# Kernel tuning notes

Hardware: AMD Instinct MI355X
Metric: run time of the kernel (lower is better)

The kernel has to match this reference:

```python
import jax, jax.numpy as jnp
import numpy as np

D = 1024   # n_embd
H = 16     # n_head
NL = 6     # n_layer
B = 16
L = 64
T = 3 * L  # interleaved (rtg, state, action) tokens
NB = 100   # rtg bucket number
DF = 4 * D


def _ln(x, g, b, eps=1e-5):
    mu = jnp.mean(x, -1, keepdims=True)
    var = jnp.mean((x - mu) ** 2, -1, keepdims=True)
    return (x - mu) * jax.lax.rsqrt(var + eps) * g + b


def _gelu(x):
    return jax.nn.gelu(x, approximate=False)  # matches torch F.gelu (erf)


def setup_inputs() -> dict:
    key = jax.random.key(0)
    ks = iter(jax.random.split(key, 64))
    def rn(shape, s=0.02):
        return jax.random.normal(next(ks), shape, jnp.float32) * s
    inp = dict(
        states=jax.random.normal(next(ks), (B, L, 91), jnp.float32),
        actions=jax.random.normal(next(ks), (B, L, 1, 27), jnp.float32),
        rtgs=jax.random.uniform(next(ks), (B, L), jnp.float32) * 100.0,
        attention_mask=jnp.ones((B, L), bool),
        y_len=L,
        # state encoder: Linear(91,D) GELU Linear(D,D) GELU
        se_w1=rn((91, D)), se_b1=jnp.zeros(D), se_w2=rn((D, D)), se_b2=jnp.zeros(D),
        # action encoder: Linear(27,D) GELU Linear(D,D)
        ae_w1=rn((27, D)), ae_b1=jnp.zeros(D), ae_w2=rn((D, D)), ae_b2=jnp.zeros(D),
        # Autodis
        ad_bucket_w=rn((1, D)), ad_bucket_b=jnp.zeros(D), ad_ret_w=rn((1, NB)), ad_res_w=rn((NB, NB)),
        pos_emb=rn((1, T, D)),
        # transformer blocks (stacked over layers)
        ln1_g=jnp.ones((NL, D)), ln1_b=jnp.zeros((NL, D)),
        Wq=rn((NL, D, D)), bq=jnp.zeros((NL, D)),
        Wk=rn((NL, D, D)), bk=jnp.zeros((NL, D)),
        Wv=rn((NL, D, D)), bv=jnp.zeros((NL, D)),
        Wp=rn((NL, D, D)), bp=jnp.zeros((NL, D)),
        ln2_g=jnp.ones((NL, D)), ln2_b=jnp.zeros((NL, D)),
        Wm1=rn((NL, D, DF)), bm1=jnp.zeros((NL, DF)),
        Wm2=rn((NL, DF, D)), bm2=jnp.zeros((NL, D)),
        lin_w=rn((D, 27)), lin_b=jnp.zeros(27),
    )
    return inp


def _forward(attention_mask, states, actions, rtgs, se_w1, se_b1, se_w2, se_b2,
             ae_w1, ae_b1, ae_w2, ae_b2, ad_bucket_w, ad_bucket_b, ad_ret_w, ad_res_w,
             pos_emb, ln1_g, ln1_b, Wq, bq, Wk, bk, Wv, bv, Wp, bp,
             ln2_g, ln2_b, Wm1, bm1, Wm2, bm2, lin_w, lin_b):
    Bsz, Ls = states.shape[0], states.shape[1]
    Ts = 3 * Ls
    hd = D // H
    # encoders
    state_emb = _gelu(_gelu(states @ se_w1 + se_b1) @ se_w2 + se_b2)          # [B,L,D]
    act = actions[:, :, 0, :]                                                  # squeeze(2) -> [B,L,27]
    action_emb = _gelu(act @ ae_w1 + ae_b1) @ ae_w2 + ae_b2                    # [B,L,D]
    # Autodis rtg embedding
    bucket_value = jnp.linspace(0.0, 100.0, NB).reshape(NB, 1)
    meta = bucket_value @ ad_bucket_w + ad_bucket_b                            # [NB,D]
    s = jax.nn.leaky_relu(rtgs[..., None] @ ad_ret_w)                          # [B,L,NB]
    s = s + s @ ad_res_w
    e = jnp.exp(s - jnp.max(s, -1, keepdims=True))
    p = e / (1e-8 + jnp.sum(e, -1, keepdims=True))
    rtg_emb = p @ meta                                                         # [B,L,D]
    # interleave rtg/state/action tokens -> [B,3L,D]
    tok = jnp.stack([rtg_emb, state_emb, action_emb], axis=2).reshape(Bsz, Ts, D)
    x = tok + pos_emb[:, :Ts]
    # combined padding + causal mask
    m = jnp.repeat(attention_mask, 3, axis=1)                                  # [B,3L]
    causal = jnp.tril(jnp.ones((Ts, Ts), bool))
    fmask = m[:, None, :, None] & m[:, None, None, :] & causal[None, None]     # [B,1,T,T]
    scale = 1.0 / np.sqrt(hd)
    for i in range(NL):
        h = _ln(x, ln1_g[i], ln1_b[i])
        q = (h @ Wq[i] + bq[i]).reshape(Bsz, Ts, H, hd).transpose(0, 2, 1, 3)
        k = (h @ Wk[i] + bk[i]).reshape(Bsz, Ts, H, hd).transpose(0, 2, 1, 3)
        v = (h @ Wv[i] + bv[i]).reshape(Bsz, Ts, H, hd).transpose(0, 2, 1, 3)
        att = jnp.einsum('bhid,bhjd->bhij', q, k) * scale
        att = jnp.where(fmask, att, -1e9)
        att = jax.nn.softmax(att, axis=-1)
        y = jnp.einsum('bhij,bhjd->bhid', att, v).transpose(0, 2, 1, 3).reshape(Bsz, Ts, D)
        x = x + (y @ Wp[i] + bp[i])
        h2 = _ln(x, ln2_g[i], ln2_b[i])
        x = x + _gelu(h2 @ Wm1[i] + bm1[i]) @ Wm2[i] + bm2[i]
    return x @ lin_w + lin_b                                                   # [B,3L,27]


def reference(states, actions, rtgs, attention_mask, y_len, se_w1, se_b1, se_w2, se_b2,
              ae_w1, ae_b1, ae_w2, ae_b2, ad_bucket_w, ad_bucket_b, ad_ret_w, ad_res_w,
              pos_emb, ln1_g, ln1_b, Wq, bq, Wk, bk, Wv, bv, Wp, bp,
              ln2_g, ln2_b, Wm1, bm1, Wm2, bm2, lin_w, lin_b):
    return _forward(attention_mask, states, actions, rtgs, se_w1, se_b1, se_w2, se_b2,
                    ae_w1, ae_b1, ae_w2, ae_b2, ad_bucket_w, ad_bucket_b, ad_ret_w, ad_res_w,
                    pos_emb, ln1_g, ln1_b, Wq, bq, Wk, bk, Wv, bv, Wp, bp,
                    ln2_g, ln2_b, Wm1, bm1, Wm2, bm2, lin_w, lin_b)
```

## Files before the change

### kernel.cpp

```cpp
#include <hip/hip_runtime.h>
#include <cmath>

typedef unsigned short u16;
typedef unsigned int   u32;
typedef short s16x8 __attribute__((ext_vector_type(8)));
typedef float f32x4 __attribute__((ext_vector_type(4)));

#define D_  1024
#define H_  16
#define NL_ 6
#define B_  16
#define L_  64
#define T_  192
#define NB_ 100
#define DF_ 4096
#define BT_ (B_*T_)
#define BL_ (B_*L_)

__device__ __forceinline__ float b2f(u16 u){ u32 x = ((u32)u)<<16; return __uint_as_float(x); }
__device__ __forceinline__ u16 f2b(float f){ u32 x = __float_as_uint(f); x += 0x7fffu + ((x>>16)&1u); return (u16)(x>>16); }
__device__ __forceinline__ float gelu_f(float v){ return 0.5f*v*(1.0f+erff(v*0.70710678118f)); }

typedef const unsigned int __attribute__((address_space(1)))* as1_u32p;
typedef unsigned int __attribute__((address_space(3)))* as3_u32p;
__device__ __forceinline__ void gload16(const void* g, void* l)
{
    __builtin_amdgcn_global_load_lds((as1_u32p)g, (as3_u32p)l, 16, 0, 0);
}

__global__ __launch_bounds__(256) void tconv_kernel(const float* __restrict__ W,
                                                    u16* __restrict__ Wt,
                                                    int K, int N,
                                                    size_t inLS, size_t outLS)
{
    __shared__ float tile[64][65];
    int tid = threadIdx.x;
    int nb = blockIdx.x * 64, kb = blockIdx.y * 64;
    const float* Wz = W + blockIdx.z * inLS;
    u16* Wtz = Wt + blockIdx.z * outLS;
    int tr = tid >> 4, tc = tid & 15;
#pragma unroll
    for (int rr = 0; rr < 4; ++rr) {
        int k = tr + rr*16;
        float4 v = *(const float4*)(Wz + (size_t)(kb + k)*N + nb + tc*4);
        tile[k][tc*4+0] = v.x; tile[k][tc*4+1] = v.y;
        tile[k][tc*4+2] = v.z; tile[k][tc*4+3] = v.w;
    }
    __syncthreads();
#pragma unroll
    for (int rr = 0; rr < 4; ++rr) {
        int n = tr + rr*16;
        ushort4 o;
        o.x = f2b(tile[tc*4+0][n]);
        o.y = f2b(tile[tc*4+1][n]);
        o.z = f2b(tile[tc*4+2][n]);
        o.w = f2b(tile[tc*4+3][n]);
        *(ushort4*)(Wtz + (size_t)(nb + n)*K + kb + tc*4) = o;
    }
}

__global__ __launch_bounds__(256) void pack_qkv_bias_kernel(const float* __restrict__ bq,
                                                            const float* __restrict__ bk,
                                                            const float* __restrict__ bv,
                                                            float* __restrict__ out)
{
    int i = blockIdx.x*256 + threadIdx.x;
    int layer = i / 3072;
    int r = i - layer*3072;
    int c = r >> 10, d = r & 1023;
    const float* src = (c == 0) ? bq : (c == 1) ? bk : bv;
    out[i] = src[layer*1024 + d];
}

__global__ __launch_bounds__(256) void tlin_kernel(const float* __restrict__ w,
                                                   float* __restrict__ wt)
{
    int k = blockIdx.x*256 + threadIdx.x;
#pragma unroll 1
    for (int c = 0; c < 27; ++c)
        wt[c*1024 + k] = w[k*27 + c];
}

__global__ __launch_bounds__(256) void embed1_kernel(const float* __restrict__ A,
                                                     const float* __restrict__ W,
                                                     const float* __restrict__ bias,
                                                     u16* __restrict__ out, int K)
{
    int idx = blockIdx.x*256 + threadIdx.x;
    int m = idx >> 10, n = idx & 1023;
    float acc = bias[n];
    for (int k = 0; k < K; ++k)
        acc += A[m*K + k] * W[k*1024 + n];
    out[idx] = f2b(gelu_f(acc));
}

__global__ __launch_bounds__(128) void rtg_kernel(const float* __restrict__ rtgs,
                                                  const float* __restrict__ ret_w,
                                                  const float* __restrict__ res_w,
                                                  const float* __restrict__ bucket_w,
                                                  const float* __restrict__ bucket_b,
                                                  float* __restrict__ eR)
{
    int r = blockIdx.x, tid = threadIdx.x;
    __shared__ float sarr[NB_];
    __shared__ float red[128];
    float rtg = rtgs[r];
    float s = 0.f;
    if (tid < NB_) {
        float v = rtg * ret_w[tid];
        s = (v > 0.f) ? v : 0.01f*v;
        sarr[tid] = s;
    }
    __syncthreads();
    float s2 = -1e30f;
    if (tid < NB_) {
        float acc = s;
        for (int m = 0; m < NB_; ++m) acc += sarr[m] * res_w[m*NB_ + tid];
        s2 = acc;
    }
    red[tid] = s2; __syncthreads();
    for (int off = 64; off > 0; off >>= 1) { if (tid < off) red[tid] = fmaxf(red[tid], red[tid+off]); __syncthreads(); }
    float mx = red[0]; __syncthreads();
    float e = (tid < NB_) ? expf(s2 - mx) : 0.f;
    red[tid] = e; __syncthreads();
    for (int off = 64; off > 0; off >>= 1) { if (tid < off) red[tid] += red[tid+off]; __syncthreads(); }
    float S = red[0]; __syncthreads();
    float bv = (100.f/99.f) * (float)tid;
    red[tid] = e * bv; __syncthreads();
    for (int off = 64; off > 0; off >>= 1) { if (tid < off) red[tid] += red[tid+off]; __syncthreads(); }
    float EB = red[0];
    float inv = 1.f/(1e-8f + S);
    float c = EB * inv, sg = S * inv;
    for (int d = tid; d < D_; d += 128)
        eR[(size_t)r*D_ + d] = c*bucket_w[d] + sg*bucket_b[d];
}

__global__ __launch_bounds__(256) void assemble_kernel(const float* __restrict__ eR,
                                                       const float* __restrict__ eS,
                                                       const float* __restrict__ eA,
                                                       const float* __restrict__ pos,
                                                       float* __restrict__ xf)
{
    int idx = blockIdx.x*256 + threadIdx.x;
    int row = idx >> 10, d = idx & 1023;
    int b = row / T_, t = row % T_;
    int l = t / 3, c = t % 3;
    const float* src = (c == 0) ? eR : (c == 1) ? eS : eA;
    xf[idx] = src[(size_t)(b*L_ + l)*D_ + d] + pos[(size_t)t*D_ + d];
}

template<int NP>
__global__ __launch_bounds__(256) void ln_kernel(const float* __restrict__ x,
                                                 const float* __restrict__ p0,
                                                 const float* __restrict__ p1,
                                                 const float* __restrict__ g,
                                                 const float* __restrict__ bb,
                                                 float* __restrict__ xout,
                                                 u16* __restrict__ out)
{
    int row = blockIdx.x, tid = threadIdx.x;
    __shared__ float rs[256], rq[256];
    float4 v = ((const float4*)(x + (size_t)row*D_))[tid];
    if (NP == 2) {
        float4 a = ((const float4*)(p0 + (size_t)row*D_))[tid];
        float4 b = ((const float4*)(p1 + (size_t)row*D_))[tid];
        v.x += a.x + b.x; v.y += a.y + b.y; v.z += a.z + b.z; v.w += a.w + b.w;
        ((float4*)(xout + (size_t)row*D_))[tid] = v;
    }
    rs[tid] = v.x+v.y+v.z+v.w;
    rq[tid] = v.x*v.x+v.y*v.y+v.z*v.z+v.w*v.w;
    __syncthreads();
    for (int off = 128; off > 0; off >>= 1) { if (tid < off){ rs[tid]+=rs[tid+off]; rq[tid]+=rq[tid+off]; } __syncthreads(); }
    float mean = rs[0]*(1.f/(float)D_);
    float var  = rq[0]*(1.f/(float)D_) - mean*mean;
    float rstd = rsqrtf(var + 1e-5f);
    int d0 = tid*4;
    ushort4 ov;
    ov.x = f2b((v.x-mean)*rstd*g[d0+0] + bb[d0+0]);
    ov.y = f2b((v.y-mean)*rstd*g[d0+1] + bb[d0+1]);
    ov.z = f2b((v.z-mean)*rstd*g[d0+2] + bb[d0+2]);
    ov.w = f2b((v.w-mean)*rstd*g[d0+3] + bb[d0+3]);
    ((ushort4*)(out + (size_t)row*D_))[tid] = ov;
}

template<int GELU_ACT, int SPLITK, int ATOMIC>
__global__ __launch_bounds__(256) void gemm_bt(const u16* __restrict__ A,
                                               const u16* __restrict__ Bt,
                                               const float* __restrict__ bias,
                                               float* __restrict__ outF,
                                               u16* __restrict__ outB,
                                               int M, int N, int K, int kc,
                                               size_t partStride)
{
    __shared__ __align__(16) u16 As[2*128*32];
    __shared__ __align__(16) u16 Bs[2*128*32];
    int tid = threadIdx.x;

    int gx = gridDim.x;
    int nwg = gx * gridDim.y;
    int id = blockIdx.y * gx + blockIdx.x;
    int q8 = nwg >> 3;
    int nid = (id & 7) * q8 + (id >> 3);
    int n0 = (nid % gx) * 128;
    int m0 = (nid / gx) * 128;

    int wave = tid >> 6, lane = tid & 63;
    int wm = (wave >> 1) * 64, wn = (wave & 1) * 64;
    int lr = lane & 15, lq = lane >> 4;
    int slotRd = (lq ^ ((lr >> 1) & 3)) * 8;

    int srow = tid >> 2;
    int sslot = (tid & 3) ^ ((srow >> 1) & 3);

    int k0 = (SPLITK > 1) ? blockIdx.z * kc : 0;
    int nIt = ((SPLITK > 1) ? kc : K) >> 5;

    const u16* ap0 = A  + (size_t)(m0 + srow) * K + k0 + sslot * 8;
    const u16* ap1 = ap0 + (size_t)64 * K;
    const u16* bp0 = Bt + (size_t)(n0 + srow) * K + k0 + sslot * 8;
    const u16* bp1 = bp0 + (size_t)64 * K;

    f32x4 acc[4][4];
#pragma unroll
    for (int i = 0; i < 4; ++i)
#pragma unroll
        for (int j = 0; j < 4; ++j) acc[i][j] = (f32x4){0.f,0.f,0.f,0.f};

    {
        u16* a0 = As + wave*512;
        u16* b0 = Bs + wave*512;
        gload16(ap0, a0); gload16(ap1, a0 + 2048);
        gload16(bp0, b0); gload16(bp1, b0 + 2048);
        ap0 += 32; ap1 += 32; bp0 += 32; bp1 += 32;
    }
    __syncthreads();

    int cur = 0;
    for (int it = 0; it < nIt; ++it) {
        if (it + 1 < nIt) {
            u16* a0 = As + (cur^1)*4096 + wave*512;
            u16* b0 = Bs + (cur^1)*4096 + wave*512;
            gload16(ap0, a0); gload16(ap1, a0 + 2048);
            gload16(bp0, b0); gload16(bp1, b0 + 2048);
            ap0 += 32; ap1 += 32; bp0 += 32; bp1 += 32;
        }
        const u16* Ac = As + cur*4096;
        const u16* Bc = Bs + cur*4096;
        s16x8 af[4], bf[4];
#pragma unroll
        for (int i = 0; i < 4; ++i)
            af[i] = *(const s16x8*)(Ac + (wm + i*16 + lr)*32 + slotRd);
#pragma unroll
        for (int j = 0; j < 4; ++j)
            bf[j] = *(const s16x8*)(Bc + (wn + j*16 + lr)*32 + slotRd);
#pragma unroll
        for (int i = 0; i < 4; ++i)
#pragma unroll
            for (int j = 0; j < 4; ++j)
                acc[i][j] = __builtin_amdgcn_mfma_f32_16x16x32_bf16(af[i], bf[j], acc[i][j], 0, 0, 0);
        __syncthreads();
        cur ^= 1;
    }

    float* outZ = (SPLITK > 1 && !ATOMIC) ? outF + (size_t)blockIdx.z * partStride : outF;
#pragma unroll
    for (int i = 0; i < 4; ++i) {
        int mbase = m0 + wm + i*16 + lq*4;
#pragma unroll
        for (int j = 0; j < 4; ++j) {
            int n = n0 + wn + j*16 + lr;
            float bvl = (SPLITK > 1) ? ((blockIdx.z == 0) ? bias[n] : 0.f) : bias[n];
#pragma unroll
            for (int r = 0; r < 4; ++r) {
                int m = mbase + r;
                float v = acc[i][j][r] + bvl;
                size_t off = (size_t)m*N + n;
                if (SPLITK > 1) {
                    if (ATOMIC) atomicAdd(outF + off, v);
                    else        outZ[off] = v;
                } else {
                    if (GELU_ACT) v = gelu_f(v);
                    if (outF) outF[off] = v;
                    if (outB) outB[off] = f2b(v);
                }
            }
        }
    }
}

__global__ __launch_bounds__(256) void attn_mfma_kernel(const u16* __restrict__ qkv,
                                                        u16* __restrict__ yb)
{
    __shared__ __align__(16) u16 Ks[192*72];
    __shared__ __align__(16) u16 Vt[64*200];
    __shared__ __align__(16) u16 Pch[4][16*40];

    int tid = threadIdx.x;
    int b = blockIdx.x >> 4, h = blockIdx.x & 15;
    int bT = b * T_;
    int colBase = h * 64;
    int w = tid >> 6, lane = tid & 63;
    int lr = lane & 15, lq = lane >> 4;
    const int S3 = 3 * D_;

#pragma unroll
    for (int it = 0; it < 6; ++it) {
        int c = it*256 + tid;
        int row = c >> 3, ch = c & 7;
        *(int4*)(Ks + row*72 + ch*8) =
            *(const int4*)(qkv + (size_t)(bT+row)*S3 + D_ + colBase + ch*8);
        union { int4 v; u16 s[8]; } rv;
        rv.v = *(const int4*)(qkv + (size_t)(bT+row)*S3 + 2*D_ + colBase + ch*8);
#pragma unroll
        for (int i2 = 0; i2 < 8; ++i2)
            Vt[(ch*8 + i2)*200 + row] = rv.s[i2];
    }
    __syncthreads();

    u16* Ch = Pch[w];

    for (int qi = 0; qi < 3; ++qi) {
        int qt = w + qi*4;
        int tqb = qt * 16;

        const u16* qrow = qkv + (size_t)(bT + tqb + lr)*S3 + colBase + lq*8;
        s16x8 af0 = *(const s16x8*)(qrow);
        s16x8 af1 = *(const s16x8*)(qrow + 32);

        f32x4 sacc[12];
#pragma unroll
        for (int jt = 0; jt < 12; ++jt) {
            if (jt <= qt) {
                s16x8 bk0 = *(const s16x8*)(Ks + (jt*16 + lr)*72 + lq*8);
                s16x8 bk1 = *(const s16x8*)(Ks + (jt*16 + lr)*72 + 32 + lq*8);
                f32x4 a = (f32x4){0.f,0.f,0.f,0.f};
                a = __builtin_amdgcn_mfma_f32_16x16x32_bf16(af0, bk0, a, 0, 0, 0);
                a = __builtin_amdgcn_mfma_f32_16x16x32_bf16(af1, bk1, a, 0, 0, 0);
                sacc[jt] = a;
            }
        }

        float mrow[4] = {-1e30f,-1e30f,-1e30f,-1e30f};
#pragma unroll
        for (int jt = 0; jt < 12; ++jt) if (jt <= qt) {
#pragma unroll
            for (int r = 0; r < 4; ++r) {
                bool valid = (jt < qt) || (lr <= lq*4 + r);
                float s = valid ? sacc[jt][r]*0.125f : -1e30f;
                sacc[jt][r] = s;
                mrow[r] = fmaxf(mrow[r], s);
            }
        }
#pragma unroll
        for (int r = 0; r < 4; ++r) {
#pragma unroll
            for (int off = 1; off < 16; off <<= 1)
                mrow[r] = fmaxf(mrow[r], __shfl_xor(mrow[r], off, 64));
        }

        float lrow[4] = {0.f,0.f,0.f,0.f};
#pragma unroll
        for (int jt = 0; jt < 12; ++jt) if (jt <= qt) {
#pragma unroll
            for (int r = 0; r < 4; ++r) {
                float e = __expf(sacc[jt][r] - mrow[r]);
                sacc[jt][r] = e;
                lrow[r] += e;
            }
        }
#pragma unroll
        for (int r = 0; r < 4; ++r) {
#pragma unroll
            for (int off = 1; off < 16; off <<= 1)
                lrow[r] += __shfl_xor(lrow[r], off, 64);
            lrow[r] = 1.f / lrow[r];
        }

        int nkt = (qt + 2) >> 1;
        f32x4 oacc[4];
#pragma unroll
        for (int nt = 0; nt < 4; ++nt) oacc[nt] = (f32x4){0.f,0.f,0.f,0.f};

#pragma unroll
        for (int kt = 0; kt < 6; ++kt) if (kt < nkt) {
            int jt0 = 2*kt, jt1 = 2*kt + 1;
#pragma unroll
            for (int r = 0; r < 4; ++r) {
                u16 e0 = f2b(sacc[jt0][r]);
                u16 e1 = (jt1 <= qt) ? f2b(sacc[jt1][r]) : (u16)0;
                Ch[(lq*4 + r)*40 + lr]      = e0;
                Ch[(lq*4 + r)*40 + 16 + lr] = e1;
            }
            s16x8 ap = *(const s16x8*)(Ch + lr*40 + lq*8);
#pragma unroll
            for (int nt = 0; nt < 4; ++nt) {
                s16x8 bv = *(const s16x8*)(Vt + (nt*16 + lr)*200 + kt*32 + lq*8);
                oacc[nt] = __builtin_amdgcn_mfma_f32_16x16x32_bf16(ap, bv, oacc[nt], 0, 0, 0);
            }
        }

#pragma unroll
        for (int nt = 0; nt < 4; ++nt)
#pragma unroll
            for (int r = 0; r < 4; ++r)
                yb[(size_t)(bT + tqb + lq*4 + r)*D_ + colBase + nt*16 + lr] =
                    f2b(oacc[nt][r] * lrow[r]);
    }
}

template<int NP>
__global__ __launch_bounds__(256) void final_kernel(const float* __restrict__ xf,
                                                    const float* __restrict__ q0,
                                                    const float* __restrict__ q1,
                                                    const float* __restrict__ lin_wT,
                                                    const float* __restrict__ lin_b,
                                                    float* __restrict__ out)
{
    int row = blockIdx.x*4 + (threadIdx.x >> 6);
    int lane = threadIdx.x & 63;
    const float4* xr = (const float4*)(xf + (size_t)row*D_);
    float4 x[4];
#pragma unroll
    for (int i = 0; i < 4; ++i) {
        float4 v = xr[lane + i*64];
        if (NP == 2) {
            float4 a = ((const float4*)(q0 + (size_t)row*D_))[lane + i*64];
            float4 b = ((const float4*)(q1 + (size_t)row*D_))[lane + i*64];
            v.x += a.x + b.x; v.y += a.y + b.y; v.z += a.z + b.z; v.w += a.w + b.w;
        }
        x[i] = v;
    }
#pragma unroll 1
    for (int c = 0; c < 27; ++c) {
        const float4* wr = (const float4*)(lin_wT + (size_t)c*D_);
        float a = 0.f;
#pragma unroll
        for (int i = 0; i < 4; ++i) {
            float4 wv = wr[lane + i*64];
            a += x[i].x*wv.x + x[i].y*wv.y + x[i].z*wv.z + x[i].w*wv.w;
        }
#pragma unroll
        for (int off = 1; off < 64; off <<= 1)
            a += __shfl_xor(a, off, 64);
        if (lane == 0) out[(size_t)row*27 + c] = a + lin_b[c];
    }
}

extern "C" void kernel_launch(void* const* d_in, const int* in_sizes, int n_in,
                              void* d_out, int out_size, void* d_ws, size_t ws_size,
                              hipStream_t stream)
{
    const float* states   = (const float*)d_in[0];
    const float* actions  = (const float*)d_in[1];
    const float* rtgs     = (const float*)d_in[2];
    const float* se_w1 = (const float*)d_in[5];
    const float* se_b1 = (const float*)d_in[6];
    const float* se_w2 = (const float*)d_in[7];
    const float* se_b2 = (const float*)d_in[8];
    const float* ae_w1 = (const float*)d_in[9];
    const float* ae_b1 = (const float*)d_in[10];
    const float* ae_w2 = (const float*)d_in[11];
    const float* ae_b2 = (const float*)d_in[12];
    const float* ad_bucket_w = (const float*)d_in[13];
    const float* ad_bucket_b = (const float*)d_in[14];
    const float* ad_ret_w = (const float*)d_in[15];
    const float* ad_res_w = (const float*)d_in[16];
    const float* pos_emb  = (const float*)d_in[17];
    const float* ln1_g = (const float*)d_in[18];
    const float* ln1_b = (const float*)d_in[19];
    const float* Wq = (const float*)d_in[20];
    const float* bq = (const float*)d_in[21];
    const float* Wk = (const float*)d_in[22];
    const float* bk = (const float*)d_in[23];
    const float* Wv = (const float*)d_in[24];
    const float* bv = (const float*)d_in[25];
    const float* Wp = (const float*)d_in[26];
    const float* bp = (const float*)d_in[27];
    const float* ln2_g = (const float*)d_in[28];
    const float* ln2_b = (const float*)d_in[29];
    const float* Wm1 = (const float*)d_in[30];
    const float* bm1 = (const float*)d_in[31];
    const float* Wm2 = (const float*)d_in[32];
    const float* bm2 = (const float*)d_in[33];
    const float* lin_w = (const float*)d_in[34];
    const float* lin_b = (const float*)d_in[35];

    char* w = (char*)d_ws;
    auto take = [&](size_t bytes) { char* p = w; w += (bytes + 255) & ~(size_t)255; return p; };

    float* xf   = (float*)take((size_t)BT_*D_*4);
    u16* hb     = (u16*)take((size_t)BT_*D_*2);
    char* qkvr  =        take((size_t)2*BT_*D_*4);
    u16*  qkvb  = (u16*)qkvr;
    float* mq0  = (float*)qkvr;
    float* mq1  = (float*)(qkvr + (size_t)BT_*D_*4);
    char* scr   =        take((size_t)BT_*DF_*2);
    u16*  midb  = (u16*)scr;
    float* pp0  = (float*)scr;
    float* pp1  = (float*)(scr + (size_t)BT_*D_*4);
    u16*  tSb   = (u16*)scr;
    u16*  tAb   = (u16*)(scr + (size_t)BL_*D_*2);
    float* eS   = (float*)(scr + (size_t)2*BL_*D_*2);
    float* eA   = (float*)(scr + (size_t)2*BL_*D_*2 + (size_t)BL_*D_*4);
    float* eR   = (float*)(scr + (size_t)2*BL_*D_*2 + (size_t)2*BL_*D_*4);

    u16* Wqkvt = (u16*)take((size_t)NL_*3*D_*D_*2);
    u16* Wpt   = (u16*)take((size_t)NL_*D_*D_*2);
    u16* Wm1t  = (u16*)take((size_t)NL_*D_*DF_*2);
    u16* Wm2t  = (u16*)take((size_t)NL_*DF_*D_*2);
    u16* sw2t  = (u16*)take((size_t)D_*D_*2);
    u16* aw2t  = (u16*)take((size_t)D_*D_*2);
    float* bqkv= (float*)take((size_t)NL_*3*D_*4);
    float* lwT = (float*)take((size_t)27*D_*4);

    size_t ask = (size_t)(w - (char*)d_ws);
    bool bigWS = (ws_size >= ask);

    const size_t PSTRIDE = (size_t)BT_*D_;

    size_t DD = (size_t)D_*D_, DDF = (size_t)D_*DF_;
    tconv_kernel<<<dim3(16,16,NL_), 256, 0, stream>>>(Wq, Wqkvt,        D_, D_, DD, 3*DD);
    tconv_kernel<<<dim3(16,16,NL_), 256, 0, stream>>>(Wk, Wqkvt + DD,   D_, D_, DD, 3*DD);
    tconv_kernel<<<dim3(16,16,NL_), 256, 0, stream>>>(Wv, Wqkvt + 2*DD, D_, D_, DD, 3*DD);
    tconv_kernel<<<dim3(16,16,NL_), 256, 0, stream>>>(Wp, Wpt,          D_, D_, DD, DD);
    tconv_kernel<<<dim3(64,16,NL_), 256, 0, stream>>>(Wm1, Wm1t, D_,  DF_, DDF, DDF);
    tconv_kernel<<<dim3(16,64,NL_), 256, 0, stream>>>(Wm2, Wm2t, DF_, D_,  DDF, DDF);
    tconv_kernel<<<dim3(16,16,1),   256, 0, stream>>>(se_w2, sw2t, D_, D_, 0, 0);
    tconv_kernel<<<dim3(16,16,1),   256, 0, stream>>>(ae_w2, aw2t, D_, D_, 0, 0);
    pack_qkv_bias_kernel<<<72, 256, 0, stream>>>(bq, bk, bv, bqkv);
    tlin_kernel<<<4, 256, 0, stream>>>(lin_w, lwT);

    embed1_kernel<<<4096, 256, 0, stream>>>(states,  se_w1, se_b1, tSb, 91);
    embed1_kernel<<<4096, 256, 0, stream>>>(actions, ae_w1, ae_b1, tAb, 27);
    gemm_bt<1,1,0><<<dim3(8,8), 256, 0, stream>>>(tSb, sw2t, se_b2, eS, nullptr, BL_, D_, D_, D_, 0);
    gemm_bt<0,1,0><<<dim3(8,8), 256, 0, stream>>>(tAb, aw2t, ae_b2, eA, nullptr, BL_, D_, D_, D_, 0);
    rtg_kernel<<<BL_, 128, 0, stream>>>(rtgs, ad_ret_w, ad_res_w, ad_bucket_w, ad_bucket_b, eR);
    assemble_kernel<<<(BT_*D_)/256, 256, 0, stream>>>(eR, eS, eA, pos_emb, xf);

    for (int i = 0; i < NL_; ++i) {
        if (i > 0 && bigWS)
            ln_kernel<2><<<BT_, 256, 0, stream>>>(xf, mq0, mq1, ln1_g + i*D_, ln1_b + i*D_, xf, hb);
        else
            ln_kernel<0><<<BT_, 256, 0, stream>>>(xf, nullptr, nullptr, ln1_g + i*D_, ln1_b + i*D_, nullptr, hb);
        gemm_bt<0,1,0><<<dim3(24,24), 256, 0, stream>>>(hb, Wqkvt + (size_t)i*3*DD, bqkv + i*3*D_,
                                                        nullptr, qkvb, BT_, 3*D_, D_, D_, 0);
        attn_mfma_kernel<<<B_*H_, 256, 0, stream>>>(qkvb, hb);
        gemm_bt<0,2,0><<<dim3(8,24,2), 256, 0, stream>>>(hb, Wpt + (size_t)i*DD, bp + i*D_,
                                                         pp0, nullptr, BT_, D_, D_, 512, PSTRIDE);
        ln_kernel<2><<<BT_, 256, 0, stream>>>(xf, pp0, pp1, ln2_g + i*D_, ln2_b + i*D_, xf, hb);
        gemm_bt<1,1,0><<<dim3(32,24), 256, 0, stream>>>(hb, Wm1t + (size_t)i*DDF, bm1 + i*DF_,
                                                        nullptr, midb, BT_, DF_, D_, D_, 0);
        if (bigWS)
            gemm_bt<0,2,0><<<dim3(8,24,2), 256, 0, stream>>>(midb, Wm2t + (size_t)i*DDF, bm2 + i*D_,
                                                             mq0, nullptr, BT_, D_, DF_, 2048, PSTRIDE);
        else
            gemm_bt<0,2,1><<<dim3(8,24,2), 256, 0, stream>>>(midb, Wm2t + (size_t)i*DDF, bm2 + i*D_,
                                                             xf, nullptr, BT_, D_, DF_, 2048, 0);
    }

    if (bigWS)
        final_kernel<2><<<BT_/4, 256, 0, stream>>>(xf, mq0, mq1, lwT, lin_b, (float*)d_out);
    else
        final_kernel<0><<<BT_/4, 256, 0, stream>>>(xf, nullptr, nullptr, lwT, lin_b, (float*)d_out);
}
```

Baseline: 1.605 ms.

## Triple-buffer GEMM loads, split attention by query chunk, shuffle LN reductions, merge transposes

The GEMM main loop moves from double to triple buffering of LDS tiles. It uses explicit vmcnt waits and a single barrier per iteration so global loads run two stages ahead of the MFMA work. The attention kernel is split over three query chunks per (batch, head) to raise block count, and each block loads only the keys and values it needs. LayerNorm reductions use wave shuffles instead of a shared-memory tree, and the four attention-weight transposes are merged into one launch. The extra LDS per GEMM block may lower occupancy, and the hand-written waitcnt depends on how the compiler orders loads.

```diff
diff --git a/kernel.cpp b/kernel.cpp
--- a/kernel.cpp
+++ b/kernel.cpp
@@ -56,6 +56,42 @@
         o.z = f2b(tile[tc*4+2][n]);
         o.w = f2b(tile[tc*4+3][n]);
         *(ushort4*)(Wtz + (size_t)(nb + n)*K + kb + tc*4) = o;
+    }
+}
+
+__global__ __launch_bounds__(256) void tconv4_kernel(const float* __restrict__ Wq,
+                                                     const float* __restrict__ Wk,
+                                                     const float* __restrict__ Wv,
+                                                     const float* __restrict__ Wp,
+                                                     u16* __restrict__ Wqkvt,
+                                                     u16* __restrict__ Wpt)
+{
+    __shared__ float tile[64][65];
+    int tid = threadIdx.x;
+    int z = blockIdx.z;
+    int sel = z / NL_, layer = z - sel*NL_;
+    size_t DD = (size_t)D_*D_;
+    const float* Wz = ((sel == 0) ? Wq : (sel == 1) ? Wk : (sel == 2) ? Wv : Wp) + layer*DD;
+    u16* Wtz = (sel == 3) ? (Wpt + layer*DD) : (Wqkvt + layer*3*DD + sel*DD);
+    int nb = blockIdx.x * 64, kb = blockIdx.y * 64;
+    int tr = tid >> 4, tc = tid & 15;
+#pragma unroll
+    for (int rr = 0; rr < 4; ++rr) {
+        int k = tr + rr*16;
+        float4 v = *(const float4*)(Wz + (size_t)(kb + k)*D_ + nb + tc*4);
+        tile[k][tc*4+0] = v.x; tile[k][tc*4+1] = v.y;
+        tile[k][tc*4+2] = v.z; tile[k][tc*4+3] = v.w;
+    }
+    __syncthreads();
+#pragma unroll
+    for (int rr = 0; rr < 4; ++rr) {
+        int n = tr + rr*16;
+        ushort4 o;
+        o.x = f2b(tile[tc*4+0][n]);
+        o.y = f2b(tile[tc*4+1][n]);
+        o.z = f2b(tile[tc*4+2][n]);
+        o.w = f2b(tile[tc*4+3][n]);
+        *(ushort4*)(Wtz + (size_t)(nb + n)*D_ + kb + tc*4) = o;
     }
 }
 
@@ -159,7 +195,8 @@
                                                  u16* __restrict__ out)
 {
     int row = blockIdx.x, tid = threadIdx.x;
-    __shared__ float rs[256], rq[256];
+    int lane = tid & 63, wv = tid >> 6;
+    __shared__ float ps[8];
     float4 v = ((const float4*)(x + (size_t)row*D_))[tid];
     if (NP == 2) {
         float4 a = ((const float4*)(p0 + (size_t)row*D_))[tid];
@@ -167,12 +204,19 @@
         v.x += a.x + b.x; v.y += a.y + b.y; v.z += a.z + b.z; v.w += a.w + b.w;
         ((float4*)(xout + (size_t)row*D_))[tid] = v;
     }
-    rs[tid] = v.x+v.y+v.z+v.w;
-    rq[tid] = v.x*v.x+v.y*v.y+v.z*v.z+v.w*v.w;
+    float s = v.x+v.y+v.z+v.w;
+    float q = v.x*v.x+v.y*v.y+v.z*v.z+v.w*v.w;
+#pragma unroll
+    for (int off = 1; off < 64; off <<= 1) {
+        s += __shfl_xor(s, off, 64);
+        q += __shfl_xor(q, off, 64);
+    }
+    if (lane == 0) { ps[wv] = s; ps[4+wv] = q; }
     __syncthreads();
-    for (int off = 128; off > 0; off >>= 1) { if (tid < off){ rs[tid]+=rs[tid+off]; rq[tid]+=rq[tid+off]; } __syncthreads(); }
-    float mean = rs[0]*(1.f/(float)D_);
-    float var  = rq[0]*(1.f/(float)D_) - mean*mean;
+    s = ps[0]+ps[1]+ps[2]+ps[3];
+    q = ps[4]+ps[5]+ps[6]+ps[7];
+    float mean = s*(1.f/(float)D_);
+    float var  = q*(1.f/(float)D_) - mean*mean;
     float rstd = rsqrtf(var + 1e-5f);
     int d0 = tid*4;
     ushort4 ov;
@@ -192,8 +236,8 @@
                                                int M, int N, int K, int kc,
                                                size_t partStride)
 {
-    __shared__ __align__(16) u16 As[2*128*32];
-    __shared__ __align__(16) u16 Bs[2*128*32];
+    __shared__ __align__(16) u16 As[3*128*32];
+    __shared__ __align__(16) u16 Bs[3*128*32];
     int tid = threadIdx.x;
 
     int gx = gridDim.x;
@@ -220,46 +264,46 @@
     const u16* bp0 = Bt + (size_t)(n0 + srow) * K + k0 + sslot * 8;
     const u16* bp1 = bp0 + (size_t)64 * K;
 
+    u16 *sA0 = As, *sA1 = As + 4096, *sA2 = As + 8192;
+    u16 *sB0 = Bs, *sB1 = Bs + 4096, *sB2 = Bs + 8192;
+    int woff = wave * 512;
+
     f32x4 acc[4][4];
 #pragma unroll
     for (int i = 0; i < 4; ++i)
 #pragma unroll
         for (int j = 0; j < 4; ++j) acc[i][j] = (f32x4){0.f,0.f,0.f,0.f};
 
-    {
-        u16* a0 = As + wave*512;
-        u16* b0 = Bs + wave*512;
-        gload16(ap0, a0); gload16(ap1, a0 + 2048);
-        gload16(bp0, b0); gload16(bp1, b0 + 2048);
-        ap0 += 32; ap1 += 32; bp0 += 32; bp1 += 32;
-    }
-    __syncthreads();
-
-    int cur = 0;
+    gload16(ap0, sA0 + woff); gload16(ap1, sA0 + 2048 + woff);
+    gload16(bp0, sB0 + woff); gload16(bp1, sB0 + 2048 + woff);
+    ap0 += 32; ap1 += 32; bp0 += 32; bp1 += 32;
+    gload16(ap0, sA1 + woff); gload16(ap1, sA1 + 2048 + woff);
+    gload16(bp0, sB1 + woff); gload16(bp1, sB1 + 2048 + woff);
+    ap0 += 32; ap1 += 32; bp0 += 32; bp1 += 32;
+
     for (int it = 0; it < nIt; ++it) {
-        if (it + 1 < nIt) {
-            u16* a0 = As + (cur^1)*4096 + wave*512;
-            u16* b0 = Bs + (cur^1)*4096 + wave*512;
-            gload16(ap0, a0); gload16(ap1, a0 + 2048);
-            gload16(bp0, b0); gload16(bp1, b0 + 2048);
+        if (it + 1 < nIt) asm volatile("s_waitcnt vmcnt(4)" ::: "memory");
+        else              asm volatile("s_waitcnt vmcnt(0)" ::: "memory");
+        asm volatile("s_barrier" ::: "memory");
+        if (it + 2 < nIt) {
+            gload16(ap0, sA2 + woff); gload16(ap1, sA2 + 2048 + woff);
+            gload16(bp0, sB2 + woff); gload16(bp1, sB2 + 2048 + woff);
             ap0 += 32; ap1 += 32; bp0 += 32; bp1 += 32;
         }
-        const u16* Ac = As + cur*4096;
-        const u16* Bc = Bs + cur*4096;
         s16x8 af[4], bf[4];
 #pragma unroll
         for (int i = 0; i < 4; ++i)
-            af[i] = *(const s16x8*)(Ac + (wm + i*16 + lr)*32 + slotRd);
+            af[i] = *(const s16x8*)(sA0 + (wm + i*16 + lr)*32 + slotRd);
 #pragma unroll
         for (int j = 0; j < 4; ++j)
-            bf[j] = *(const s16x8*)(Bc + (wn + j*16 + lr)*32 + slotRd);
+            bf[j] = *(const s16x8*)(sB0 + (wn + j*16 + lr)*32 + slotRd);
 #pragma unroll
         for (int i = 0; i < 4; ++i)
 #pragma unroll
             for (int j = 0; j < 4; ++j)
                 acc[i][j] = __builtin_amdgcn_mfma_f32_16x16x32_bf16(af[i], bf[j], acc[i][j], 0, 0, 0);
-        __syncthreads();
-        cur ^= 1;
+        u16* t0 = sA0; sA0 = sA1; sA1 = sA2; sA2 = t0;
+        u16* t1 = sB0; sB0 = sB1; sB1 = sB2; sB2 = t1;
     }
 
     float* outZ = (SPLITK > 1 && !ATOMIC) ? outF + (size_t)blockIdx.z * partStride : outF;
@@ -297,16 +341,17 @@
 
     int tid = threadIdx.x;
     int b = blockIdx.x >> 4, h = blockIdx.x & 15;
+    int c = blockIdx.y;
+    int nrows = (c + 1) * 64;
     int bT = b * T_;
     int colBase = h * 64;
     int w = tid >> 6, lane = tid & 63;
     int lr = lane & 15, lq = lane >> 4;
     const int S3 = 3 * D_;
 
-#pragma unroll
-    for (int it = 0; it < 6; ++it) {
-        int c = it*256 + tid;
-        int row = c >> 3, ch = c & 7;
+    for (int it = 0; it < (nrows >> 5); ++it) {
+        int cc = it*256 + tid;
+        int row = cc >> 3, ch = cc & 7;
         *(int4*)(Ks + row*72 + ch*8) =
             *(const int4*)(qkv + (size_t)(bT+row)*S3 + D_ + colBase + ch*8);
         union { int4 v; u16 s[8]; } rv;
@@ -318,94 +363,91 @@
     __syncthreads();
 
     u16* Ch = Pch[w];
-
-    for (int qi = 0; qi < 3; ++qi) {
-        int qt = w + qi*4;
-        int tqb = qt * 16;
-
-        const u16* qrow = qkv + (size_t)(bT + tqb + lr)*S3 + colBase + lq*8;
-        s16x8 af0 = *(const s16x8*)(qrow);
-        s16x8 af1 = *(const s16x8*)(qrow + 32);
-
-        f32x4 sacc[12];
-#pragma unroll
-        for (int jt = 0; jt < 12; ++jt) {
-            if (jt <= qt) {
-                s16x8 bk0 = *(const s16x8*)(Ks + (jt*16 + lr)*72 + lq*8);
-                s16x8 bk1 = *(const s16x8*)(Ks + (jt*16 + lr)*72 + 32 + lq*8);
-                f32x4 a = (f32x4){0.f,0.f,0.f,0.f};
-                a = __builtin_amdgcn_mfma_f32_16x16x32_bf16(af0, bk0, a, 0, 0, 0);
-                a = __builtin_amdgcn_mfma_f32_16x16x32_bf16(af1, bk1, a, 0, 0, 0);
-                sacc[jt] = a;
-            }
-        }
-
-        float mrow[4] = {-1e30f,-1e30f,-1e30f,-1e30f};
-#pragma unroll
-        for (int jt = 0; jt < 12; ++jt) if (jt <= qt) {
-#pragma unroll
-            for (int r = 0; r < 4; ++r) {
-                bool valid = (jt < qt) || (lr <= lq*4 + r);
-                float s = valid ? sacc[jt][r]*0.125f : -1e30f;
-                sacc[jt][r] = s;
-                mrow[r] = fmaxf(mrow[r], s);
-            }
-        }
+    int qt = c*4 + w;
+    int tqb = qt * 16;
+
+    const u16* qrow = qkv + (size_t)(bT + tqb + lr)*S3 + colBase + lq*8;
+    s16x8 af0 = *(const s16x8*)(qrow);
+    s16x8 af1 = *(const s16x8*)(qrow + 32);
+
+    f32x4 sacc[12];
+#pragma unroll
+    for (int jt = 0; jt < 12; ++jt) {
+        if (jt <= qt) {
+            s16x8 bk0 = *(const s16x8*)(Ks + (jt*16 + lr)*72 + lq*8);
+            s16x8 bk1 = *(const s16x8*)(Ks + (jt*16 + lr)*72 + 32 + lq*8);
+            f32x4 a = (f32x4){0.f,0.f,0.f,0.f};
+            a = __builtin_amdgcn_mfma_f32_16x16x32_bf16(af0, bk0, a, 0, 0, 0);
+            a = __builtin_amdgcn_mfma_f32_16x16x32_bf16(af1, bk1, a, 0, 0, 0);
+            sacc[jt] = a;
+        }
+    }
+
+    float mrow[4] = {-1e30f,-1e30f,-1e30f,-1e30f};
+#pragma unroll
+    for (int jt = 0; jt < 12; ++jt) if (jt <= qt) {
 #pragma unroll
         for (int r = 0; r < 4; ++r) {
-#pragma unroll
-            for (int off = 1; off < 16; off <<= 1)
-                mrow[r] = fmaxf(mrow[r], __shfl_xor(mrow[r], off, 64));
-        }
-
-        float lrow[4] = {0.f,0.f,0.f,0.f};
-#pragma unroll
-        for (int jt = 0; jt < 12; ++jt) if (jt <= qt) {
-#pragma unroll
-            for (int r = 0; r < 4; ++r) {
-                float e = __expf(sacc[jt][r] - mrow[r]);
-                sacc[jt][r] = e;
-                lrow[r] += e;
-            }
-        }
+            bool valid = (jt < qt) || (lr <= lq*4 + r);
+            float s = valid ? sacc[jt][r]*0.125f : -1e30f;
+            sacc[jt][r] = s;
+            mrow[r] = fmaxf(mrow[r], s);
+        }
+    }
+#pragma unroll
+    for (int r = 0; r < 4; ++r) {
+#pragma unroll
+        for (int off = 1; off < 16; off <<= 1)
+            mrow[r] = fmaxf(mrow[r], __shfl_xor(mrow[r], off, 64));
+    }
+
+    float lrow[4] = {0.f,0.f,0.f,0.f};
+#pragma unroll
+    for (int jt = 0; jt < 12; ++jt) if (jt <= qt) {
 #pragma unroll
         for (int r = 0; r < 4; ++r) {
-#pragma unroll
-            for (int off = 1; off < 16; off <<= 1)
-                lrow[r] += __shfl_xor(lrow[r], off, 64);
-            lrow[r] = 1.f / lrow[r];
-        }
-
-        int nkt = (qt + 2) >> 1;
-        f32x4 oacc[4];
-#pragma unroll
-        for (int nt = 0; nt < 4; ++nt) oacc[nt] = (f32x4){0.f,0.f,0.f,0.f};
-
-#pragma unroll
-        for (int kt = 0; kt < 6; ++kt) if (kt < nkt) {
-            int jt0 = 2*kt, jt1 = 2*kt + 1;
-#pragma unroll
-            for (int r = 0; r < 4; ++r) {
-                u16 e0 = f2b(sacc[jt0][r]);
-                u16 e1 = (jt1 <= qt) ? f2b(sacc[jt1][r]) : (u16)0;
-                Ch[(lq*4 + r)*40 + lr]      = e0;
-                Ch[(lq*4 + r)*40 + 16 + lr] = e1;
-            }
-            s16x8 ap = *(const s16x8*)(Ch + lr*40 + lq*8);
-#pragma unroll
-            for (int nt = 0; nt < 4; ++nt) {
-                s16x8 bv = *(const s16x8*)(Vt + (nt*16 + lr)*200 + kt*32 + lq*8);
-                oacc[nt] = __builtin_amdgcn_mfma_f32_16x16x32_bf16(ap, bv, oacc[nt], 0, 0, 0);
-            }
-        }
-
-#pragma unroll
-        for (int nt = 0; nt < 4; ++nt)
-#pragma unroll
-            for (int r = 0; r < 4; ++r)
-                yb[(size_t)(bT + tqb + lq*4 + r)*D_ + colBase + nt*16 + lr] =
-                    f2b(oacc[nt][r] * lrow[r]);
-    }
+            float e = __expf(sacc[jt][r] - mrow[r]);
+            sacc[jt][r] = e;
+            lrow[r] += e;
+        }
+    }
+#pragma unroll
+    for (int r = 0; r < 4; ++r) {
+#pragma unroll
+        for (int off = 1; off < 16; off <<= 1)
+            lrow[r] += __shfl_xor(lrow[r], off, 64);
+        lrow[r] = 1.f / lrow[r];
+    }
+
+    int nkt = (qt + 2) >> 1;
+    f32x4 oacc[4];
+#pragma unroll
+    for (int nt = 0; nt < 4; ++nt) oacc[nt] = (f32x4){0.f,0.f,0.f,0.f};
+
+#pragma unroll
+    for (int kt = 0; kt < 6; ++kt) if (kt < nkt) {
+        int jt0 = 2*kt, jt1 = 2*kt + 1;
+#pragma unroll
+        for (int r = 0; r < 4; ++r) {
+            u16 e0 = f2b(sacc[jt0][r]);
+            u16 e1 = (jt1 <= qt) ? f2b(sacc[jt1][r]) : (u16)0;
+            Ch[(lq*4 + r)*40 + lr]      = e0;
+            Ch[(lq*4 + r)*40 + 16 + lr] = e1;
+        }
+        s16x8 ap = *(const s16x8*)(Ch + lr*40 + lq*8);
+#pragma unroll
+        for (int nt = 0; nt < 4; ++nt) {
+            s16x8 bv = *(const s16x8*)(Vt + (nt*16 + lr)*200 + kt*32 + lq*8);
+            oacc[nt] = __builtin_amdgcn_mfma_f32_16x16x32_bf16(ap, bv, oacc[nt], 0, 0, 0);
+        }
+    }
+
+#pragma unroll
+    for (int nt = 0; nt < 4; ++nt)
+#pragma unroll
+        for (int r = 0; r < 4; ++r)
+            yb[(size_t)(bT + tqb + lq*4 + r)*D_ + colBase + nt*16 + lr] =
+                f2b(oacc[nt][r] * lrow[r]);
 }
 
 template<int NP>
@@ -519,10 +561,7 @@
     const size_t PSTRIDE = (size_t)BT_*D_;
 
     size_t DD = (size_t)D_*D_, DDF = (size_t)D_*DF_;
-    tconv_kernel<<<dim3(16,16,NL_), 256, 0, stream>>>(Wq, Wqkvt,        D_, D_, DD, 3*DD);
-    tconv_kernel<<<dim3(16,16,NL_), 256, 0, stream>>>(Wk, Wqkvt + DD,   D_, D_, DD, 3*DD);
-    tconv_kernel<<<dim3(16,16,NL_), 256, 0, stream>>>(Wv, Wqkvt + 2*DD, D_, D_, DD, 3*DD);
-    tconv_kernel<<<dim3(16,16,NL_), 256, 0, stream>>>(Wp, Wpt,          D_, D_, DD, DD);
+    tconv4_kernel<<<dim3(16,16,4*NL_), 256, 0, stream>>>(Wq, Wk, Wv, Wp, Wqkvt, Wpt);
     tconv_kernel<<<dim3(64,16,NL_), 256, 0, stream>>>(Wm1, Wm1t, D_,  DF_, DDF, DDF);
     tconv_kernel<<<dim3(16,64,NL_), 256, 0, stream>>>(Wm2, Wm2t, DF_, D_,  DDF, DDF);
     tconv_kernel<<<dim3(16,16,1),   256, 0, stream>>>(se_w2, sw2t, D_, D_, 0, 0);
@@ -544,7 +583,7 @@
             ln_kernel<0><<<BT_, 256, 0, stream>>>(xf, nullptr, nullptr, ln1_g + i*D_, ln1_b + i*D_, nullptr, hb);
         gemm_bt<0,1,0><<<dim3(24,24), 256, 0, stream>>>(hb, Wqkvt + (size_t)i*3*DD, bqkv + i*3*D_,
                                                         nullptr, qkvb, BT_, 3*D_, D_, D_, 0);
-        attn_mfma_kernel<<<B_*H_, 256, 0, stream>>>(qkvb, hb);
+        attn_mfma_kernel<<<dim3(B_*H_,3), 256, 0, stream>>>(qkvb, hb);
         gemm_bt<0,2,0><<<dim3(8,24,2), 256, 0, stream>>>(hb, Wpt + (size_t)i*DD, bp + i*D_,
                                                          pp0, nullptr, BT_, D_, D_, 512, PSTRIDE);
         ln_kernel<2><<<BT_, 256, 0, stream>>>(xf, pp0, pp1, ln2_g + i*D_, ln2_b + i*D_, xf, hb);
```

Measured after the change: 1.597 ms. Within noise of the previous version (-0.5%).
